# Optimization experiments

Measured on AMD Instinct MI355X. Metric: run time of the kernel, lower is better.

Reference implementation:

```python
import jax, jax.numpy as jnp
import numpy as np
import math

B, S, D, H, W = 4, 8192, 1024, 16, 512  # batch, seq, d_model, heads, attention_window
HD = D // H


def setup_inputs() -> dict:
    key = jax.random.key(0)
    ks = jax.random.split(key, 5)
    scale = 0.02
    return {
        "x": jax.random.normal(ks[0], (B, S, D), dtype=jnp.float32),
        "wq": jax.random.normal(ks[1], (D, D), dtype=jnp.float32) * scale,
        "bq": jnp.zeros((D,), dtype=jnp.float32),
        "wk": jax.random.normal(ks[2], (D, D), dtype=jnp.float32) * scale,
        "bk": jnp.zeros((D,), dtype=jnp.float32),
        "wv": jax.random.normal(ks[3], (D, D), dtype=jnp.float32) * scale,
        "bv": jnp.zeros((D,), dtype=jnp.float32),
        "wo": jax.random.normal(ks[4], (D, D), dtype=jnp.float32) * scale,
        "bo": jnp.zeros((D,), dtype=jnp.float32),
    }


def reference(x, wq, bq, wk, bk, wv, bv, wo, bo):
    # torch Linear: y = x @ W.T + b
    q = (x @ wq.T + bq).reshape(B, S, H, HD)
    k = (x @ wk.T + bk).reshape(B, S, H, HD)
    v = (x @ wv.T + bv).reshape(B, S, H, HD)

    nb = S // W  # number of query blocks
    qb = q.reshape(B, nb, W, H, HD)

    # pad keys/values by W at the front so every block sees a 2W key window
    kp = jnp.pad(k, ((0, 0), (W, 0), (0, 0), (0, 0)))
    vp = jnp.pad(v, ((0, 0), (W, 0), (0, 0), (0, 0)))
    # padded key indices for block n: [n*W, n*W + 2W) <-> original [n*W - W, n*W + W)
    idx = jnp.arange(nb)[:, None] * W + jnp.arange(2 * W)[None, :]  # [nb, 2W]
    kb = kp[:, idx]  # [B, nb, 2W, H, HD]
    vb = vp[:, idx]  # [B, nb, 2W, H, HD]

    scores = jnp.einsum('bnqhd,bnkhd->bnhqk', qb, kb) / math.sqrt(HD)
    valid = (idx >= W)  # padded (out-of-range) keys only occur for block 0
    scores = jnp.where(valid[None, :, None, None, :], scores, -jnp.inf)
    attn = jax.nn.softmax(scores, axis=-1)  # softmax over the block's key window

    out = jnp.einsum('bnhqk,bnkhd->bnqhd', attn, vb).reshape(B, S, D)
    return out @ wo.T + bo
```

## Files before the change

kernel.cpp:

```cpp
#include <hip/hip_runtime.h>
#include <hip/hip_bf16.h>
#include <cstdint>

typedef __bf16 bf16;
typedef __attribute__((ext_vector_type(8))) __bf16 bf16x8;
typedef __attribute__((ext_vector_type(4))) __bf16 bf16x4;
typedef __attribute__((ext_vector_type(4))) float f32x4;
typedef __attribute__((ext_vector_type(16))) float f32x16;
typedef __attribute__((ext_vector_type(4))) unsigned int u32x4;

#define B_ 4
#define S_ 8192
#define D_ 1024
#define H_ 16
#define HD_ 64
#define W_ 512
#define M_ (B_*S_)

#define EXP2F(x) __builtin_amdgcn_exp2f(x)
#define MFMA16(a,b,c) __builtin_amdgcn_mfma_f32_16x16x32_bf16(a,b,c,0,0,0)
#define MFMA32(a,b,c) __builtin_amdgcn_mfma_f32_32x32x16_bf16(a,b,c,0,0,0)

__device__ __forceinline__ void async16(const void* g, void* l) {
  __builtin_amdgcn_global_load_lds(
      (const __attribute__((address_space(1))) unsigned int*)g,
      (__attribute__((address_space(3))) unsigned int*)l, 16, 0, 0);
}

__device__ __forceinline__ void cast_region(const float* __restrict__ in,
                                            bf16* __restrict__ out, int n4,
                                            int i0, int stride) {
  for (int i = i0; i < n4; i += stride) {
    f32x4 v = ((const f32x4*)in)[i];
    bf16x4 o = { (bf16)v[0], (bf16)v[1], (bf16)v[2], (bf16)v[3] };
    ((bf16x4*)out)[i] = o;
  }
}

__global__ void cast_all(const float* __restrict__ x,  bf16* __restrict__ xb,
                         const float* __restrict__ wq, bf16* __restrict__ wqb,
                         const float* __restrict__ wk, bf16* __restrict__ wkb,
                         const float* __restrict__ wv, bf16* __restrict__ wvb,
                         const float* __restrict__ wo, bf16* __restrict__ wob) {
  int i0 = blockIdx.x * blockDim.x + threadIdx.x;
  int stride = gridDim.x * blockDim.x;
  cast_region(x,  xb,  M_*D_/4, i0, stride);
  cast_region(wq, wqb, D_*D_/4, i0, stride);
  cast_region(wk, wkb, D_*D_/4, i0, stride);
  cast_region(wv, wvb, D_*D_/4, i0, stride);
  cast_region(wo, wob, D_*D_/4, i0, stride);
}

template<int MODE>
__global__ void __launch_bounds__(512, 2) gemm_bt(
    const bf16* __restrict__ A, const bf16* __restrict__ Bw,
    const float* __restrict__ bias, void* __restrict__ outp, float scale)
{
  constexpr int K = D_, N = D_;
  __shared__ char lds[3 * 32768];
  int bid = blockIdx.x;
  int nid = (bid & 7) * 64 + (bid >> 3);
  int bm = nid >> 2, bn = nid & 3;
  const int tid = threadIdx.x, lane = tid & 63;
  const int w = tid >> 6, wr = w >> 2, wc = w & 3;
  f32x4 acc[8][4] = {};
  const int sR  = ((tid >> 6) * 16) + (tid & 15);
  const int skb = ((tid >> 4) & 3) * 16;
  const char* Ab = (const char*)(A + (size_t)bm * 256 * K);
  const char* Bb = (const char*)(Bw + (size_t)bn * 256 * K);

  auto stageA = [&](int t2, int h) {
    char* dst = lds + (t2 % 3) * 32768 + h * 8192 + tid * 16;
    async16(Ab + (size_t)(h * 128 + sR) * (K * 2) + t2 * 64 + skb, dst);
  };
  auto stageB = [&](int t2, int h) {
    char* dst = lds + (t2 % 3) * 32768 + 16384 + h * 8192 + tid * 16;
    async16(Bb + (size_t)(h * 128 + sR) * (K * 2) + t2 * 64 + skb, dst);
  };

  stageA(0, 0); stageB(0, 0); stageA(0, 1); stageB(0, 1);
  stageA(1, 0); stageB(1, 0); stageA(1, 1); stageB(1, 1);
  asm volatile("s_waitcnt vmcnt(4)" ::: "memory");
  __builtin_amdgcn_s_barrier();

#pragma unroll 1
  for (int t = 0; t < 32; ++t) {
    const char* base = lds + (t % 3) * 32768;
    const char* baseB = base + 16384;
    bool pre = (t < 30);
    if (pre) { stageA(t + 2, 0); stageB(t + 2, 0); }
    bf16x8 a[4], b[4];
#pragma unroll
    for (int mi = 0; mi < 4; ++mi)
      a[mi] = *(const bf16x8*)(base + (wr * 8 + mi) * 1024 + lane * 16);
#pragma unroll
    for (int ni = 0; ni < 4; ++ni)
      b[ni] = *(const bf16x8*)(baseB + (wc * 4 + ni) * 1024 + lane * 16);
    __builtin_amdgcn_s_barrier();
    asm volatile("s_waitcnt lgkmcnt(0)" ::: "memory");
    __builtin_amdgcn_sched_barrier(0);
    __builtin_amdgcn_s_setprio(1);
#pragma unroll
    for (int mi = 0; mi < 4; ++mi)
#pragma unroll
      for (int ni = 0; ni < 4; ++ni)
        acc[mi][ni] = MFMA16(a[mi], b[ni], acc[mi][ni]);
    __builtin_amdgcn_s_setprio(0);
    __builtin_amdgcn_s_barrier();
    if (pre) { stageA(t + 2, 1); stageB(t + 2, 1); }
    bf16x8 a2[4];
#pragma unroll
    for (int mi = 0; mi < 4; ++mi)
      a2[mi] = *(const bf16x8*)(base + (wr * 8 + 4 + mi) * 1024 + lane * 16);
    __builtin_amdgcn_s_barrier();
    asm volatile("s_waitcnt lgkmcnt(0)" ::: "memory");
    __builtin_amdgcn_sched_barrier(0);
    __builtin_amdgcn_s_setprio(1);
#pragma unroll
    for (int mi = 0; mi < 4; ++mi)
#pragma unroll
      for (int ni = 0; ni < 4; ++ni)
        acc[4 + mi][ni] = MFMA16(a2[mi], b[ni], acc[4 + mi][ni]);
    __builtin_amdgcn_s_setprio(0);
    if (pre) {
      asm volatile("s_waitcnt vmcnt(4)" ::: "memory");
    } else {
      asm volatile("s_waitcnt vmcnt(0)" ::: "memory");
    }
    __builtin_amdgcn_s_barrier();
  }

  int row0 = bm * 256 + wr * 128, col0 = bn * 256 + wc * 64;
  int rsub = (lane >> 4) * 4;
#pragma unroll
  for (int ni = 0; ni < 4; ++ni) {
    int col = col0 + ni * 16 + (lane & 15);
    float bz = bias[col];
#pragma unroll
    for (int mi = 0; mi < 8; ++mi) {
#pragma unroll
      for (int r = 0; r < 4; ++r) {
        int row = row0 + mi * 16 + rsub + r;
        float v = (acc[mi][ni][r] + bz) * scale;
        if (MODE == 0) {
          ((bf16*)outp)[(size_t)row * N + col] = (bf16)v;
        } else if (MODE == 1) {
          ((bf16*)outp)[((size_t)(row >> 13) * D_ + col) * S_ + (row & (S_-1))] = (bf16)v;
        } else {
          ((float*)outp)[(size_t)row * N + col] = v;
        }
      }
    }
  }
}

__global__ void __launch_bounds__(256, 3) attn_kernel(
    const bf16* __restrict__ Q, const bf16* __restrict__ Kb,
    const bf16* __restrict__ Vt, bf16* __restrict__ Ao)
{
  __shared__ char Klds[3][8192];
  __shared__ char Vlds[3][8192];
  int x = blockIdx.x;
  int qt = (x >> 3) & 3;
  int g  = (x & 7) + 8 * (x >> 5);
  int h = g & 15, n = (g >> 4) & 15, b = g >> 8;
  int tid = threadIdx.x, lane = tid & 63, w = tid >> 6;
  int hi = lane >> 5, qv = lane & 31;
  int qrow = n * W_ + qt * 128 + w * 32;

  const bf16* Qrow = Q + ((size_t)(b * S_ + qrow + qv)) * D_ + h * 64;
  bf16x8 Qf[4];
#pragma unroll
  for (int s = 0; s < 4; ++s) Qf[s] = *(const bf16x8*)(Qrow + s * 16 + hi * 8);

  const bf16* Kg = Kb + ((size_t)b * S_) * D_ + h * 64;
  const bf16* Vg = Vt + ((size_t)(b * H_ + h) * HD_) * S_;

  const int srow = tid >> 3;
  const int sseg = (tid & 7) ^ (srow & 7);
  const int fswq = (qv & 7) << 4;

  f32x16 O0 = {}, O1 = {};
  float l_r = 0.f;

  const int c0 = (n == 0) ? 8 : 0;
  const int ksbase = (n - 1) * W_;

  auto stage = [&](int c) {
    int ks = ksbase + c * 64;
    int so = (c % 3) * 8192;
    const bf16* kr = Kg + (size_t)(ks + srow) * D_ + sseg * 8;
    async16(kr,                    &Klds[0][0] + so + tid * 16);
    async16(kr + 32 * D_,          &Klds[0][0] + so + 4096 + tid * 16);
    const bf16* vr = Vg + (size_t)srow * S_ + ks + sseg * 8;
    async16(vr,                    &Vlds[0][0] + so + tid * 16);
    async16(vr + (size_t)32 * S_,  &Vlds[0][0] + so + 4096 + tid * 16);
  };

  stage(c0);
  stage(c0 + 1);
  asm volatile("s_waitcnt vmcnt(4)" ::: "memory");
  __builtin_amdgcn_s_barrier();

  for (int c = c0; c < 16; ++c) {
    bool pre = (c + 2 < 16);
    if (pre) stage(c + 2);
    const char* kbuf = &Klds[0][0] + (c % 3) * 8192;
    const char* vbuf = &Vlds[0][0] + (c % 3) * 8192;
    f32x16 C0 = {}, C1 = {};
    __builtin_amdgcn_s_setprio(1);
#pragma unroll
    for (int s = 0; s < 4; ++s) {
      bf16x8 k0 = *(const bf16x8*)(kbuf + qv * 128        + ((s * 32 + hi * 16) ^ fswq));
      bf16x8 k1 = *(const bf16x8*)(kbuf + (32 + qv) * 128 + ((s * 32 + hi * 16) ^ fswq));
      C0 = MFMA32(k0, Qf[s], C0);
      C1 = MFMA32(k1, Qf[s], C1);
    }
    __builtin_amdgcn_s_setprio(0);
    float p0[16], p1[16];
#pragma unroll
    for (int r = 0; r < 16; ++r) {
      p0[r] = EXP2F(C0[r]);
      p1[r] = EXP2F(C1[r]);
    }
    float q0[8], q1[4];
#pragma unroll
    for (int i = 0; i < 8; ++i)
      q0[i] = (p0[2*i] + p0[2*i+1]) + (p1[2*i] + p1[2*i+1]);
#pragma unroll
    for (int i = 0; i < 4; ++i) q1[i] = q0[2*i] + q0[2*i+1];
    l_r += (q1[0] + q1[1]) + (q1[2] + q1[3]);
    unsigned int L0[8], L1[8];
#pragma unroll
    for (int t = 0; t < 8; ++t) {
      asm("v_cvt_pk_bf16_f32 %0, %1, %2" : "=v"(L0[t]) : "v"(p0[2*t]), "v"(p0[2*t+1]));
      asm("v_cvt_pk_bf16_f32 %0, %1, %2" : "=v"(L1[t]) : "v"(p1[2*t]), "v"(p1[2*t+1]));
    }
    asm volatile("v_permlane32_swap_b32 %0, %1" : "+v"(L0[0]), "+v"(L0[2]));
    asm volatile("v_permlane32_swap_b32 %0, %1" : "+v"(L0[1]), "+v"(L0[3]));
    asm volatile("v_permlane32_swap_b32 %0, %1" : "+v"(L0[4]), "+v"(L0[6]));
    asm volatile("v_permlane32_swap_b32 %0, %1" : "+v"(L0[5]), "+v"(L0[7]));
    asm volatile("v_permlane32_swap_b32 %0, %1" : "+v"(L1[0]), "+v"(L1[2]));
    asm volatile("v_permlane32_swap_b32 %0, %1" : "+v"(L1[1]), "+v"(L1[3]));
    asm volatile("v_permlane32_swap_b32 %0, %1" : "+v"(L1[4]), "+v"(L1[6]));
    asm volatile("v_permlane32_swap_b32 %0, %1" : "+v"(L1[5]), "+v"(L1[7]));
    u32x4 F[2][2];
    F[0][0] = u32x4{L0[0], L0[1], L0[2], L0[3]};
    F[0][1] = u32x4{L0[4], L0[5], L0[6], L0[7]};
    F[1][0] = u32x4{L1[0], L1[1], L1[2], L1[3]};
    F[1][1] = u32x4{L1[4], L1[5], L1[6], L1[7]};
    __builtin_amdgcn_s_setprio(1);
#pragma unroll
    for (int T = 0; T < 2; ++T)
#pragma unroll
      for (int s = 0; s < 2; ++s) {
        bf16x8 pf = *(bf16x8*)&F[T][s];
        int kbyteoff = T * 64 + s * 32 + hi * 16;
        bf16x8 v0 = *(const bf16x8*)(vbuf + qv * 128        + (kbyteoff ^ fswq));
        bf16x8 v1 = *(const bf16x8*)(vbuf + (32 + qv) * 128 + (kbyteoff ^ fswq));
        O0 = MFMA32(v0, pf, O0);
        O1 = MFMA32(v1, pf, O1);
      }
    __builtin_amdgcn_s_setprio(0);
    if (pre) {
      asm volatile("s_waitcnt vmcnt(4)" ::: "memory");
    } else {
      asm volatile("s_waitcnt vmcnt(0)" ::: "memory");
    }
    __builtin_amdgcn_s_barrier();
  }
  float lt = l_r + __shfl_xor(l_r, 32);
  float inv = 1.0f / lt;
  size_t obase = ((size_t)(b * S_ + qrow + qv)) * D_ + h * 64;
#pragma unroll
  for (int ot = 0; ot < 2; ++ot) {
#pragma unroll
    for (int rq = 0; rq < 4; ++rq) {
      int hd = ot * 32 + 8 * rq + 4 * hi;
      bf16x4 ov;
#pragma unroll
      for (int j = 0; j < 4; ++j) {
        float val = (ot == 0 ? O0[rq*4 + j] : O1[rq*4 + j]) * inv;
        ov[j] = (bf16)val;
      }
      *(bf16x4*)(Ao + obase + hd) = ov;
    }
  }
}

extern "C" void kernel_launch(void* const* d_in, const int* in_sizes, int n_in,
                              void* d_out, int out_size, void* d_ws, size_t ws_size,
                              hipStream_t stream) {
  const float* x  = (const float*)d_in[0];
  const float* wq = (const float*)d_in[1];
  const float* bq = (const float*)d_in[2];
  const float* wk = (const float*)d_in[3];
  const float* bk = (const float*)d_in[4];
  const float* wv = (const float*)d_in[5];
  const float* bv = (const float*)d_in[6];
  const float* wo = (const float*)d_in[7];
  const float* bo = (const float*)d_in[8];
  float* out = (float*)d_out;

  char* ws = (char*)d_ws;
  const size_t sz = (size_t)M_ * D_ * 2;
  bf16* xb  = (bf16*)(ws + 0*sz);
  bf16* qb  = (bf16*)(ws + 1*sz);
  bf16* kb  = (bf16*)(ws + 2*sz);
  bf16* vt  = (bf16*)(ws + 3*sz);
  bf16* ao  = (bf16*)(ws + 4*sz);
  bf16* wqb = (bf16*)(ws + 5*sz);
  bf16* wkb = wqb + (size_t)D_*D_;
  bf16* wvb = wkb + (size_t)D_*D_;
  bf16* wob = wvb + (size_t)D_*D_;

  cast_all<<<2048, 256, 0, stream>>>(x, xb, wq, wqb, wk, wkb, wv, wvb, wo, wob);

  gemm_bt<0><<<512, 512, 0, stream>>>(xb, wqb, bq, qb, 0.125f * 1.44269504f);
  gemm_bt<0><<<512, 512, 0, stream>>>(xb, wkb, bk, kb, 1.0f);
  gemm_bt<1><<<512, 512, 0, stream>>>(xb, wvb, bv, vt, 1.0f);

  attn_kernel<<<4096, 256, 0, stream>>>(qb, kb, vt, ao);

  gemm_bt<2><<<512, 512, 0, stream>>>(ao, wob, bo, out, 1.0f);
}
```

Measured before the change: 551.0 us.

## Software-pipeline QK of next chunk with softmax and drop GEMM inner barriers

The attention loop now computes the QK^T MFMAs for chunk c+1 before the exp2, bf16 pack and PV work of chunk c. This lets matrix-core work overlap the VALU softmax work. The per-iteration wait moves to the loop top and becomes a full vmcnt(0) wait before staging chunk c+2, which shortens how far global loads run ahead. In the projection GEMM, the mid-iteration s_barrier, lgkmcnt waits and sched_barriers are removed, leaving the compiler to order LDS reads and MFMAs. That trades explicit synchronisation for scheduling freedom and relies on the triple-buffered layout staying race-free.

```diff
diff --git a/kernel.cpp b/kernel.cpp
--- a/kernel.cpp
+++ b/kernel.cpp
@@ -96,9 +96,6 @@
 #pragma unroll
     for (int ni = 0; ni < 4; ++ni)
       b[ni] = *(const bf16x8*)(baseB + (wc * 4 + ni) * 1024 + lane * 16);
-    __builtin_amdgcn_s_barrier();
-    asm volatile("s_waitcnt lgkmcnt(0)" ::: "memory");
-    __builtin_amdgcn_sched_barrier(0);
     __builtin_amdgcn_s_setprio(1);
 #pragma unroll
     for (int mi = 0; mi < 4; ++mi)
@@ -106,15 +103,11 @@
       for (int ni = 0; ni < 4; ++ni)
         acc[mi][ni] = MFMA16(a[mi], b[ni], acc[mi][ni]);
     __builtin_amdgcn_s_setprio(0);
-    __builtin_amdgcn_s_barrier();
     if (pre) { stageA(t + 2, 1); stageB(t + 2, 1); }
     bf16x8 a2[4];
 #pragma unroll
     for (int mi = 0; mi < 4; ++mi)
       a2[mi] = *(const bf16x8*)(base + (wr * 8 + 4 + mi) * 1024 + lane * 16);
-    __builtin_amdgcn_s_barrier();
-    asm volatile("s_waitcnt lgkmcnt(0)" ::: "memory");
-    __builtin_amdgcn_sched_barrier(0);
     __builtin_amdgcn_s_setprio(1);
 #pragma unroll
     for (int mi = 0; mi < 4; ++mi)
@@ -197,44 +190,45 @@
     async16(vr + (size_t)32 * S_,  &Vlds[0][0] + so + 4096 + tid * 16);
   };
 
+  auto QK = [&](int c, f32x16& A0, f32x16& A1) {
+    const char* kbuf = &Klds[0][0] + (c % 3) * 8192;
+    __builtin_amdgcn_s_setprio(1);
+#pragma unroll
+    for (int s = 0; s < 4; ++s) {
+      bf16x8 k0 = *(const bf16x8*)(kbuf + qv * 128        + ((s * 32 + hi * 16) ^ fswq));
+      bf16x8 k1 = *(const bf16x8*)(kbuf + (32 + qv) * 128 + ((s * 32 + hi * 16) ^ fswq));
+      A0 = MFMA32(k0, Qf[s], A0);
+      A1 = MFMA32(k1, Qf[s], A1);
+    }
+    __builtin_amdgcn_s_setprio(0);
+  };
+
   stage(c0);
   stage(c0 + 1);
   asm volatile("s_waitcnt vmcnt(4)" ::: "memory");
   __builtin_amdgcn_s_barrier();
-
+  f32x16 C0 = {}, C1 = {};
+  QK(c0, C0, C1);
+
+#pragma unroll 1
   for (int c = c0; c < 16; ++c) {
-    bool pre = (c + 2 < 16);
-    if (pre) stage(c + 2);
-    const char* kbuf = &Klds[0][0] + (c % 3) * 8192;
-    const char* vbuf = &Vlds[0][0] + (c % 3) * 8192;
-    f32x16 C0 = {}, C1 = {};
-    __builtin_amdgcn_s_setprio(1);
-#pragma unroll
-    for (int s = 0; s < 4; ++s) {
-      bf16x8 k0 = *(const bf16x8*)(kbuf + qv * 128        + ((s * 32 + hi * 16) ^ fswq));
-      bf16x8 k1 = *(const bf16x8*)(kbuf + (32 + qv) * 128 + ((s * 32 + hi * 16) ^ fswq));
-      C0 = MFMA32(k0, Qf[s], C0);
-      C1 = MFMA32(k1, Qf[s], C1);
-    }
-    __builtin_amdgcn_s_setprio(0);
-    float p0[16], p1[16];
-#pragma unroll
-    for (int r = 0; r < 16; ++r) {
-      p0[r] = EXP2F(C0[r]);
-      p1[r] = EXP2F(C1[r]);
-    }
-    float q0[8], q1[4];
+    asm volatile("s_waitcnt vmcnt(0)" ::: "memory");
+    __builtin_amdgcn_s_barrier();
+    if (c + 2 < 16) stage(c + 2);
+    f32x16 N0 = {}, N1 = {};
+    if (c + 1 < 16) QK(c + 1, N0, N1);
+#pragma unroll
+    for (int r = 0; r < 16; ++r) { C0[r] = EXP2F(C0[r]); C1[r] = EXP2F(C1[r]); }
+    float q0[8];
 #pragma unroll
     for (int i = 0; i < 8; ++i)
-      q0[i] = (p0[2*i] + p0[2*i+1]) + (p1[2*i] + p1[2*i+1]);
-#pragma unroll
-    for (int i = 0; i < 4; ++i) q1[i] = q0[2*i] + q0[2*i+1];
-    l_r += (q1[0] + q1[1]) + (q1[2] + q1[3]);
+      q0[i] = (C0[2*i] + C0[2*i+1]) + (C1[2*i] + C1[2*i+1]);
+    l_r += ((q0[0] + q0[1]) + (q0[2] + q0[3])) + ((q0[4] + q0[5]) + (q0[6] + q0[7]));
     unsigned int L0[8], L1[8];
 #pragma unroll
     for (int t = 0; t < 8; ++t) {
-      asm("v_cvt_pk_bf16_f32 %0, %1, %2" : "=v"(L0[t]) : "v"(p0[2*t]), "v"(p0[2*t+1]));
-      asm("v_cvt_pk_bf16_f32 %0, %1, %2" : "=v"(L1[t]) : "v"(p1[2*t]), "v"(p1[2*t+1]));
+      asm("v_cvt_pk_bf16_f32 %0, %1, %2" : "=v"(L0[t]) : "v"(C0[2*t]), "v"(C0[2*t+1]));
+      asm("v_cvt_pk_bf16_f32 %0, %1, %2" : "=v"(L1[t]) : "v"(C1[2*t]), "v"(C1[2*t+1]));
     }
     asm volatile("v_permlane32_swap_b32 %0, %1" : "+v"(L0[0]), "+v"(L0[2]));
     asm volatile("v_permlane32_swap_b32 %0, %1" : "+v"(L0[1]), "+v"(L0[3]));
@@ -249,6 +243,7 @@
     F[0][1] = u32x4{L0[4], L0[5], L0[6], L0[7]};
     F[1][0] = u32x4{L1[0], L1[1], L1[2], L1[3]};
     F[1][1] = u32x4{L1[4], L1[5], L1[6], L1[7]};
+    const char* vbuf = &Vlds[0][0] + (c % 3) * 8192;
     __builtin_amdgcn_s_setprio(1);
 #pragma unroll
     for (int T = 0; T < 2; ++T)
@@ -262,12 +257,7 @@
         O1 = MFMA32(v1, pf, O1);
       }
     __builtin_amdgcn_s_setprio(0);
-    if (pre) {
-      asm volatile("s_waitcnt vmcnt(4)" ::: "memory");
-    } else {
-      asm volatile("s_waitcnt vmcnt(0)" ::: "memory");
-    }
-    __builtin_amdgcn_s_barrier();
+    C0 = N0; C1 = N1;
   }
   float lt = l_r + __shfl_xor(l_r, 32);
   float inv = 1.0f / lt;
```

Measured after the change: 553.0 us. No clear change (+0.4%).
